# Kernel optimization log

Hardware: AMD Instinct MI355X
Metric: run time of the kernel (lower is better)

The kernel has to match this reference:

```python
import jax, jax.numpy as jnp
import numpy as np

B, C = 256, 1024
EPS = 1e-5
N_LAYERS = 3


def setup_inputs() -> dict:
    key = jax.random.key(0)
    ks = jax.random.split(key, 8)
    x = jax.random.normal(ks[0], (B, C, 7, 7), dtype=jnp.float32)
    # BatchNorm affine params per layer
    bn_gamma = 1.0 + 0.1 * jax.random.normal(ks[1], (N_LAYERS, C), dtype=jnp.float32)
    bn_beta = 0.1 * jax.random.normal(ks[2], (N_LAYERS, C), dtype=jnp.float32)
    # 1x1 conv weights [layer, out_c, in_c] and biases
    conv_w = jax.random.normal(ks[3], (N_LAYERS, C, C), dtype=jnp.float32) / np.sqrt(C)
    conv_b = 0.1 * jax.random.normal(ks[4], (N_LAYERS, C), dtype=jnp.float32)
    # prediction heads: 4 directions x 3 steps, torch Linear convention W:[out,in]
    lin_w = jax.random.normal(ks[5], (4, 3, C, C), dtype=jnp.float32) / np.sqrt(C)
    lin_b = 0.1 * jax.random.normal(ks[6], (4, 3, C), dtype=jnp.float32)
    return dict(x=x, bn_gamma=bn_gamma, bn_beta=bn_beta,
                conv_w=conv_w, conv_b=conv_b, lin_w=lin_w, lin_b=lin_b)


def _contexts(x, bn_gamma, bn_beta, conv_w, conv_b):
    # gather all 25 3x3 patches: [25, B, C, 3, 3]
    h = jnp.stack([x[:, :, y:y + 3, xx:xx + 3]
                   for y in range(5) for xx in range(5)])
    for l in range(N_LAYERS):
        # BatchNorm2d (training mode): stats over batch + spatial, per patch slice
        mean = h.mean(axis=(1, 3, 4), keepdims=True)
        var = ((h - mean) ** 2).mean(axis=(1, 3, 4), keepdims=True)
        g = bn_gamma[l][None, None, :, None, None]
        b = bn_beta[l][None, None, :, None, None]
        h = (h - mean) * jax.lax.rsqrt(var + EPS) * g + b
        h = jax.nn.relu(h)
        # 1x1 conv == per-pixel matmul over channels
        h = jnp.einsum('pbchw,oc->pbohw', h, conv_w[l]) \
            + conv_b[l][None, None, :, None, None]
    # adaptive avg pool to 1x1, squeeze -> [25, B, C]
    return h.mean(axis=(3, 4))


def reference(x, bn_gamma, bn_beta, conv_w, conv_b, lin_w, lin_b):
    ctx = _contexts(x, bn_gamma, bn_beta, conv_w, conv_b)  # [25, B, C]

    def lin(c, d, s):
        return jnp.einsum('bc,oc->bo', c, lin_w[d, s]) + lin_b[d, s]

    preds = []
    for y1 in range(5):
        for x1 in range(5):
            y2, x2 = y1 + 2, x1 + 2
            c = ctx[y1 * 5 + x1]
            if y2 in (2, 3):
                for s in range(3):
                    if y2 + s + 1 > 6:
                        break
                    preds.append(lin(c, 0, s))
            if y1 in (3, 4):
                for s in range(3):
                    if y1 - (s + 1) < 0:
                        break
                    preds.append(lin(c, 1, s))
            if x2 in (2, 3):
                for s in range(3):
                    if x2 + s + 1 > 6:
                        break
                    preds.append(lin(c, 2, s))
            if x1 in (3, 4):
                for s in range(3):
                    if x1 - (s + 1) < 0:
                        break
                    preds.append(lin(c, 3, s))
    return jnp.stack(preds)  # [120, B, C]
```

## Files before the change

### kernel.cpp

```cpp
#include <hip/hip_runtime.h>
#include <hip/hip_bf16.h>
#include <stdint.h>

#define BB 256
#define CC 1024
#define NP 25
#define EPS 1e-5f

typedef __attribute__((ext_vector_type(8))) short bf16x8;
typedef __attribute__((ext_vector_type(4))) float f32x4;
typedef unsigned int u32;

#define MFMA16(A, B, C) __builtin_amdgcn_mfma_f32_16x16x32_bf16(A, B, C, 0, 0, 0)

__device__ __forceinline__ void gload16(const u32* g, u32* l)
{
  __builtin_amdgcn_global_load_lds(
      (const __attribute__((address_space(1))) u32*)g,
      (__attribute__((address_space(3))) u32*)l, 16, 0, 0);
}


__device__ __forceinline__ void head_entry(int j, int* pp, int* ww)
{
  int cnt = 0;
  for (int y1 = 0; y1 < 5; y1++)
    for (int x1 = 0; x1 < 5; x1++) {
      int p = y1 * 5 + x1;
      int y2 = y1 + 2, x2 = x1 + 2;
      if (y2 == 2 || y2 == 3)
        for (int s = 0; s < 3; s++) { if (y2 + s + 1 > 6) break; if (cnt == j) { *pp = p; *ww = 0 + s; return; } cnt++; }
      if (y1 == 3 || y1 == 4)
        for (int s = 0; s < 3; s++) { if (y1 - (s + 1) < 0) break; if (cnt == j) { *pp = p; *ww = 3 + s; return; } cnt++; }
      if (x2 == 2 || x2 == 3)
        for (int s = 0; s < 3; s++) { if (x2 + s + 1 > 6) break; if (cnt == j) { *pp = p; *ww = 6 + s; return; } cnt++; }
      if (x1 == 3 || x1 == 4)
        for (int s = 0; s < 3; s++) { if (x1 - (s + 1) < 0) break; if (cnt == j) { *pp = p; *ww = 9 + s; return; } cnt++; }
    }
}

__device__ __forceinline__ u32 rne_hi(u32 x)
{
  return (x + 0x7FFFu + ((x >> 16) & 1u)) & 0xFFFF0000u;
}

__device__ __forceinline__ u32 rne_pack(float a, float b)
{
  return (rne_hi(__float_as_uint(a)) >> 16) | rne_hi(__float_as_uint(b));
}

__device__ __forceinline__ float bflo(u32 u) { return __uint_as_float(u << 16); }
__device__ __forceinline__ float bfhi(u32 u) { return __uint_as_float(u & 0xFFFF0000u); }


__global__ void k_xsums(const float* __restrict__ x, float* __restrict__ xs1,
                        float* __restrict__ xs2)
{
  int pos = blockIdx.x * 256 + threadIdx.x;
  float s1 = 0.f, s2 = 0.f;
  for (int b = 0; b < BB; b++) {
    float v = x[(size_t)b * 50176 + pos];
    s1 += v; s2 = fmaf(v, v, s2);
  }
  xs1[pos] = s1; xs2[pos] = s2;
}

__global__ void k_stats1(const float* __restrict__ xs1, const float* __restrict__ xs2,
                         const float* __restrict__ gam, const float* __restrict__ bet,
                         float* __restrict__ ssc, float* __restrict__ ssh)
{
  int p = blockIdx.x;
  int c = blockIdx.y * 256 + threadIdx.x;
  int y1 = p / 5, x1 = p % 5;
  float s1 = 0.f, s2 = 0.f;
  for (int dy = 0; dy < 3; dy++)
    for (int dx = 0; dx < 3; dx++) {
      int pos = c * 49 + (y1 + dy) * 7 + (x1 + dx);
      s1 += xs1[pos]; s2 += xs2[pos];
    }
  const float inv = 1.0f / 2304.0f;
  float mean = s1 * inv;
  float var  = s2 * inv - mean * mean;
  float rs   = rsqrtf(var + EPS);
  float sc   = rs * gam[c];
  ssc[(size_t)p * CC + c] = sc;
  ssh[(size_t)p * CC + c] = bet[c] - mean * sc;
}


__global__ void k_tsplit(const float* __restrict__ x,
                         const float* __restrict__ ssc, const float* __restrict__ ssh,
                         u32* __restrict__ bufS, int pbase, int pcount)
{
  __shared__ float tile[128][51];
  int b = blockIdx.x, cg = blockIdx.y;
  const float* src = x + (size_t)b * 50176 + (size_t)cg * 128 * 49;
  for (int idx = threadIdx.x; idx < 6272; idx += 256)
    tile[idx / 49][idx % 49] = src[idx];
  __syncthreads();
  const int t = threadIdx.x;
  const int u = t & 63;
  const int segs = pcount * 9;
  for (int sg = t >> 6; sg < segs; sg += 4) {
    int pl = sg / 9, yx = sg - pl * 9;
    int p = pbase + pl;
    int pos = (p / 5 + yx / 3) * 7 + (p % 5) + (yx % 3);
    int c0 = cg * 128 + u * 2;
    float2 sc = *(const float2*)(ssc + (size_t)p * CC + c0);
    float2 sh = *(const float2*)(ssh + (size_t)p * CC + c0);
    float v0 = fmaxf(fmaf(tile[u * 2][pos],     sc.x, sh.x), 0.f);
    float v1 = fmaxf(fmaf(tile[u * 2 + 1][pos], sc.y, sh.y), 0.f);
    bufS[((size_t)pl * 2304 + b * 9 + yx) * 512 + cg * 64 + u] = rne_pack(v0, v1);
  }
}


__global__ void k_wsplit_rn(const float* __restrict__ w, u32* __restrict__ dst, int total)
{
  int g = blockIdx.x * 256 + threadIdx.x;
  if (g >= total) return;
  int row = g >> 9;
  int idx = g & 511;
  const float* src = w + ((size_t)row << 10) + 2 * idx;
  dst[g] = rne_pack(src[0], src[1]);
}


__global__ void k_absplit(const u32* __restrict__ src,
                          const float* __restrict__ ssc, const float* __restrict__ ssh,
                          u32* __restrict__ dst, int pbase)
{
  int r = blockIdx.x * 8 + (threadIdx.x >> 5);
  int slab = threadIdx.x & 31;
  int pg = pbase + r / 2304;
  const u32* su = src + (size_t)r * 512 + slab * 16;
  const float* scp = ssc + (size_t)pg * CC + slab * 32;
  const float* shp = ssh + (size_t)pg * CC + slab * 32;
  u32 hi[16];
  #pragma unroll
  for (int j = 0; j < 8; j++) {
    u32 p0 = su[2 * j], p1 = su[2 * j + 1];
    float4 f = { bflo(p0), bfhi(p0), bflo(p1), bfhi(p1) };
    float4 s = *(const float4*)(scp + 4 * j);
    float4 h = *(const float4*)(shp + 4 * j);
    f.x = fmaxf(fmaf(f.x, s.x, h.x), 0.f);
    f.y = fmaxf(fmaf(f.y, s.y, h.y), 0.f);
    f.z = fmaxf(fmaf(f.z, s.z, h.z), 0.f);
    f.w = fmaxf(fmaf(f.w, s.w, h.w), 0.f);
    hi[2 * j]     = rne_pack(f.x, f.y);
    hi[2 * j + 1] = rne_pack(f.z, f.w);
  }
  u32* op = dst + (size_t)r * 512 + slab * 16;
  *(uint4*)(op + 0)  = make_uint4(hi[0], hi[1], hi[2], hi[3]);
  *(uint4*)(op + 4)  = make_uint4(hi[4], hi[5], hi[6], hi[7]);
  *(uint4*)(op + 8)  = make_uint4(hi[8], hi[9], hi[10], hi[11]);
  *(uint4*)(op + 12) = make_uint4(hi[12], hi[13], hi[14], hi[15]);
}


__global__ void k_statsfin(const float* __restrict__ part, const float* __restrict__ gam,
                           const float* __restrict__ bet, float* __restrict__ ssc,
                           float* __restrict__ ssh, int pbase)
{
  int pl = blockIdx.x;
  int c  = blockIdx.y * 256 + threadIdx.x;
  float s1 = 0.f, s2 = 0.f;
  for (int mb = 0; mb < 18; mb++) {
    const float* pp = part + ((size_t)(pl * 18 + mb) * CC + c) * 2;
    s1 += pp[0]; s2 += pp[1];
  }
  const float inv = 1.0f / 2304.0f;
  float mean = s1 * inv;
  float var  = s2 * inv - mean * mean;
  float rs   = rsqrtf(var + EPS);
  float sc   = rs * gam[c];
  int pg = pbase + pl;
  ssc[(size_t)pg * CC + c] = sc;
  ssh[(size_t)pg * CC + c] = bet[c] - mean * sc;
}


__global__ void k_pool(const u32* __restrict__ h, const float* __restrict__ ssc,
                       const float* __restrict__ ssh, u32* __restrict__ apool, int pbase)
{
  int row = blockIdx.x;
  int pl = row >> 8;
  int pg = pbase + pl;
  int c = threadIdx.x * 4;
  float4 sc = *(const float4*)(ssc + (size_t)pg * CC + c);
  float4 sh = *(const float4*)(ssh + (size_t)pg * CC + c);
  const u32* hp = h + (size_t)row * 9 * 512 + (c >> 1);
  float4 s = {0.f, 0.f, 0.f, 0.f};
  #pragma unroll
  for (int yx = 0; yx < 9; yx++) {
    uint2 pp = *(const uint2*)(hp + (size_t)yx * 512);
    float4 v = { bflo(pp.x), bfhi(pp.x), bflo(pp.y), bfhi(pp.y) };
    s.x += fmaxf(fmaf(v.x, sc.x, sh.x), 0.f);
    s.y += fmaxf(fmaf(v.y, sc.y, sh.y), 0.f);
    s.z += fmaxf(fmaf(v.z, sc.z, sh.z), 0.f);
    s.w += fmaxf(fmaf(v.w, sc.w, sh.w), 0.f);
  }
  const float inv9 = 1.0f / 9.0f;
  uint2 o = { rne_pack(s.x * inv9, s.y * inv9), rne_pack(s.z * inv9, s.w * inv9) };
  u32* op = apool + ((size_t)(pbase * 256) + row) * 512 + (c >> 1);
  *(uint2*)op = o;
}


template<int OUT, bool STATS>
__device__ __forceinline__ void mg_body(
    const u32* __restrict__ Agl, const u32* __restrict__ Bp,
    const float* __restrict__ bias, void* __restrict__ Cptr,
    int m0, int n0, float* __restrict__ partOut, int mb)
{
  __shared__ u32 sA[2][128 * 16];
  __shared__ u32 sB[2][128 * 16];

  const int t = threadIdx.x;
  const int l = t & 63, wv = t >> 6;
  const int lr = l & 15, lk = l >> 4;
  const int wm = (wv >> 1) * 64, wn = (wv & 1) * 64;

  int fAh[4], fBh[4];
  #pragma unroll
  for (int i = 0; i < 4; i++) {
    int Ra = wm + i * 16 + lr;
    int Rb = wn + i * 16 + lr;
    fAh[i] = Ra * 16 + ((lk ^ ((Ra >> 1) & 3)) << 2);
    fBh[i] = Rb * 16 + ((lk ^ ((Rb >> 1) & 3)) << 2);
  }

  int grow[2], gg[2], gdst[2];
  #pragma unroll
  for (int q = 0; q < 2; q++) {
    int rr = wv * 32 + q * 16 + (l >> 2);
    grow[q] = rr;
    gg[q] = (((l & 3) ^ ((rr >> 1) & 3)) << 2);
    gdst[q] = (wv * 32 + q * 16) * 16;
  }
  const u32* Brow = Bp + (size_t)n0 * 512;
  const u32* Agr  = Agl + (size_t)m0 * 512;

  f32x4 acc[4][4];
  #pragma unroll
  for (int i = 0; i < 4; i++)
    #pragma unroll
    for (int j = 0; j < 4; j++) { f32x4 z = {0.f, 0.f, 0.f, 0.f}; acc[i][j] = z; }

  #pragma unroll
  for (int q = 0; q < 2; q++) {
    gload16(Brow + (size_t)grow[q] * 512 + gg[q], &sB[0][gdst[q]]);
    gload16(Agr + (size_t)grow[q] * 512 + gg[q], &sA[0][gdst[q]]);
  }
  __syncthreads();

  #pragma unroll 1
  for (int it = 0; it < 32; ++it) {
    const int cur = it & 1, nxt = cur ^ 1;
    const bool pf = (it < 31);
    if (pf) {
      const int so = (it + 1) << 4;
      #pragma unroll
      for (int q = 0; q < 2; q++) {
        gload16(Brow + (size_t)grow[q] * 512 + so + gg[q], &sB[nxt][gdst[q]]);
        gload16(Agr + (size_t)grow[q] * 512 + so + gg[q], &sA[nxt][gdst[q]]);
      }
    }
    bf16x8 Ah[4], Bh[4];
    #pragma unroll
    for (int i = 0; i < 4; i++) {
      Ah[i] = *(const bf16x8*)&sA[cur][fAh[i]];
      Bh[i] = *(const bf16x8*)&sB[cur][fBh[i]];
    }
    #pragma unroll
    for (int i = 0; i < 4; i++)
      #pragma unroll
      for (int j = 0; j < 4; j++)
        acc[i][j] = MFMA16(Ah[i], Bh[j], acc[i][j]);
    __syncthreads();
  }

  float* Cf = (float*)Cptr;
  u32*   Cu = (u32*)Cptr;
  float st1[4], st2[4];
  #pragma unroll
  for (int j = 0; j < 4; j++) { st1[j] = 0.f; st2[j] = 0.f; }
  #pragma unroll
  for (int j = 0; j < 4; j++) {
    int ocol = n0 + wn + j * 16 + lr;
    float bj = bias[ocol];
    #pragma unroll
    for (int i = 0; i < 4; i++) {
      int orow = m0 + wm + i * 16 + lk * 4;
      #pragma unroll
      for (int reg = 0; reg < 4; reg++) {
        float v = acc[i][j][reg] + bj;
        if (STATS) { st1[j] += v; st2[j] = fmaf(v, v, st2[j]); }
        int row = orow + reg;
        if (OUT == 0) {
          Cf[(size_t)row * CC + ocol] = v;
        } else {
          float pv = __shfl_xor(v, 1);
          if (!(lr & 1))
            Cu[(size_t)row * 512 + (ocol >> 1)] = rne_pack(v, pv);
        }
      }
    }
  }
  if (STATS) {
    float* srb = (float*)&sA[0][0];
    #pragma unroll
    for (int j = 0; j < 4; j++) {
      st1[j] += __shfl_xor(st1[j], 16, 64);
      st1[j] += __shfl_xor(st1[j], 32, 64);
      st2[j] += __shfl_xor(st2[j], 16, 64);
      st2[j] += __shfl_xor(st2[j], 32, 64);
    }
    if (lk == 0) {
      #pragma unroll
      for (int j = 0; j < 4; j++) {
        srb[wv * 64 + j * 16 + lr]       = st1[j];
        srb[256 + wv * 64 + j * 16 + lr] = st2[j];
      }
    }
    __syncthreads();
    if (t < 128) {
      int ch = t >> 6, c6 = t & 63;
      float a1 = srb[ch * 64 + c6] + srb[(ch + 2) * 64 + c6];
      float a2 = srb[256 + ch * 64 + c6] + srb[256 + (ch + 2) * 64 + c6];
      float2 o = { a1, a2 };
      *(float2*)(partOut + ((size_t)mb * CC + n0 + t) * 2) = o;
    }
  }
}

#define SWZ_G 64

template<int OUT, bool STATS>
__global__ __launch_bounds__(256, 2)
void k_mg(const u32* __restrict__ A, const u32* __restrict__ Bp,
          const float* __restrict__ bias, void* __restrict__ Cptr,
          int mtiles, float* __restrict__ partOut)
{
  int id = blockIdx.y * gridDim.x + blockIdx.x;
  int g = id / (SWZ_G * 8);
  int rem = id - g * (SWZ_G * 8);
  int gsz = mtiles - g * SWZ_G; if (gsz > SWZ_G) gsz = SWZ_G;
  int mt = g * SWZ_G + rem % gsz;
  int nt = rem / gsz;
  mg_body<OUT, STATS>(A, Bp, bias, Cptr, mt * 128, nt * 128, partOut, mt);
}

__global__ __launch_bounds__(256, 2)
void k_heads(const u32* __restrict__ ctxp, const u32* __restrict__ wplh,
             const float* __restrict__ lb, float* __restrict__ out)
{
  int p, w;
  head_entry(blockIdx.y, &p, &w);
  mg_body<0, false>(ctxp + (size_t)p * BB * 512,
                    wplh + (size_t)w * 524288,
                    lb + (size_t)w * CC,
                    out + (size_t)blockIdx.y * BB * CC,
                    (blockIdx.x >> 3) * 128, (blockIdx.x & 7) * 128,
                    nullptr, 0);
}


extern "C" void kernel_launch(void* const* d_in, const int* in_sizes, int n_in,
                              void* d_out, int out_size, void* d_ws, size_t ws_size,
                              hipStream_t stream)
{
  const float* x   = (const float*)d_in[0];
  const float* bng = (const float*)d_in[1];
  const float* bnb = (const float*)d_in[2];
  const float* cw  = (const float*)d_in[3];
  const float* cb  = (const float*)d_in[4];
  const float* lw  = (const float*)d_in[5];
  const float* lb  = (const float*)d_in[6];
  float* out = (float*)d_out;

  const size_t W = ws_size / 4;
  const size_t SZ_WHI  = 3ull * 524288;
  const size_t SZ_WPL  = 12ull * 524288;
  const size_t SZ_PS   = 6400ull * 512;
  const size_t SZ_CTXP = 6400ull * 512;
  const size_t SZ_XS   = 50176;
  const size_t SZ_SS   = 25ull * 1024;

  auto need = [&](int pc) -> size_t {
    return SZ_WHI + SZ_WPL
         + 2ull * pc * 2304 * 512
         + SZ_PS + SZ_CTXP + 2 * SZ_XS + 2 * SZ_SS
         + (size_t)pc * 18 * 1024 * 2;
  };
  int PC;
  if      (W >= need(25)) PC = 25;
  else if (W >= need(5))  PC = 5;
  else                    PC = 1;

  u32*   whi    = (u32*)d_ws;
  u32*   wpl    = whi + SZ_WHI;
  u32*   bufS   = wpl + SZ_WPL;
  u32*   bufO   = bufS + (size_t)PC * 2304 * 512;
  u32*   pooledS= bufO + (size_t)PC * 2304 * 512;
  u32*   ctxp   = pooledS + SZ_PS;
  float* xs1    = (float*)(ctxp + SZ_CTXP);
  float* xs2    = xs1 + SZ_XS;
  float* ssc    = xs2 + SZ_XS;
  float* ssh    = ssc + SZ_SS;
  float* part   = ssh + SZ_SS;

  k_wsplit_rn<<<(int)(SZ_WHI / 256), 256, 0, stream>>>(cw, whi, (int)SZ_WHI);
  k_wsplit_rn<<<(int)(SZ_WPL / 256), 256, 0, stream>>>(lw, wpl, (int)SZ_WPL);
  k_xsums<<<196, 256, 0, stream>>>(x, xs1, xs2);
  k_stats1<<<dim3(25, 4), 256, 0, stream>>>(xs1, xs2, bng, bnb, ssc, ssh);

  for (int pbase = 0; pbase < NP; pbase += PC) {
    const int rows = PC * 2304;
    const int mtiles = PC * 18;
    const dim3 gconv(mtiles, 8);
    k_tsplit<<<dim3(256, 8), 256, 0, stream>>>(x, ssc, ssh, bufS, pbase, PC);
    k_mg<1, true><<<gconv, 256, 0, stream>>>(bufS, whi, cb, bufO, mtiles, part);
    k_statsfin<<<dim3(PC, 4), 256, 0, stream>>>(part, bng + CC, bnb + CC, ssc, ssh, pbase);
    k_absplit<<<rows / 8, 256, 0, stream>>>(bufO, ssc, ssh, bufS, pbase);
    k_mg<1, true><<<gconv, 256, 0, stream>>>(bufS, whi + 524288, cb + CC,
                                             bufO, mtiles, part);
    k_statsfin<<<dim3(PC, 4), 256, 0, stream>>>(part, bng + 2 * CC, bnb + 2 * CC, ssc, ssh, pbase);
    k_pool<<<PC * 256, 256, 0, stream>>>(bufO, ssc, ssh, pooledS, pbase);
  }

  k_mg<1, false><<<dim3(50, 8), 256, 0, stream>>>(pooledS, whi + 2 * 524288,
                                                  cb + 2 * CC, ctxp, 50, nullptr);
  k_heads<<<dim3(16, 120), 256, 0, stream>>>(ctxp, wpl, lb, out);
}
```

Measured before the change: 635.2 us.

## Enlarge conv GEMM tile to 256x128 with 512-thread blocks

Replaces the 128x128 conv GEMM kernel with a 512-thread, 8-wave variant that covers 256 rows per block. Each B (weight) tile loaded into LDS is now reused across twice as many A rows, which cuts weight traffic and halves the number of blocks. The BatchNorm partial-statistics reduction is rewritten to sum over four M-waves, and `k_statsfin` now reads 9 partials per patch instead of 18. The heads GEMM keeps the old 128x128 body. The trade-offs are a larger LDS footprint per block, fewer blocks to fill the GPU, and register pressure from `launch_bounds(512,4)`.

```diff
diff --git a/kernel.cpp b/kernel.cpp
--- a/kernel.cpp
+++ b/kernel.cpp
@@ -165,8 +165,8 @@
   int pl = blockIdx.x;
   int c  = blockIdx.y * 256 + threadIdx.x;
   float s1 = 0.f, s2 = 0.f;
-  for (int mb = 0; mb < 18; mb++) {
-    const float* pp = part + ((size_t)(pl * 18 + mb) * CC + c) * 2;
+  for (int mb = 0; mb < 9; mb++) {
+    const float* pp = part + ((size_t)(pl * 9 + mb) * CC + c) * 2;
     s1 += pp[0]; s2 += pp[1];
   }
   const float inv = 1.0f / 2304.0f;
@@ -207,11 +207,10 @@
 }
 
 
-template<int OUT, bool STATS>
 __device__ __forceinline__ void mg_body(
     const u32* __restrict__ Agl, const u32* __restrict__ Bp,
-    const float* __restrict__ bias, void* __restrict__ Cptr,
-    int m0, int n0, float* __restrict__ partOut, int mb)
+    const float* __restrict__ bias, float* __restrict__ Cf,
+    int m0, int n0)
 {
   __shared__ u32 sA[2][128 * 16];
   __shared__ u32 sB[2][128 * 16];
@@ -229,7 +228,6 @@
     fAh[i] = Ra * 16 + ((lk ^ ((Ra >> 1) & 3)) << 2);
     fBh[i] = Rb * 16 + ((lk ^ ((Rb >> 1) & 3)) << 2);
   }
-
   int grow[2], gg[2], gdst[2];
   #pragma unroll
   for (int q = 0; q < 2; q++) {
@@ -257,8 +255,7 @@
   #pragma unroll 1
   for (int it = 0; it < 32; ++it) {
     const int cur = it & 1, nxt = cur ^ 1;
-    const bool pf = (it < 31);
-    if (pf) {
+    if (it < 31) {
       const int so = (it + 1) << 4;
       #pragma unroll
       for (int q = 0; q < 2; q++) {
@@ -280,11 +277,6 @@
     __syncthreads();
   }
 
-  float* Cf = (float*)Cptr;
-  u32*   Cu = (u32*)Cptr;
-  float st1[4], st2[4];
-  #pragma unroll
-  for (int j = 0; j < 4; j++) { st1[j] = 0.f; st2[j] = 0.f; }
   #pragma unroll
   for (int j = 0; j < 4; j++) {
     int ocol = n0 + wn + j * 16 + lr;
@@ -293,17 +285,116 @@
     for (int i = 0; i < 4; i++) {
       int orow = m0 + wm + i * 16 + lk * 4;
       #pragma unroll
+      for (int reg = 0; reg < 4; reg++)
+        Cf[(size_t)(orow + reg) * CC + ocol] = acc[i][j][reg] + bj;
+    }
+  }
+}
+
+__global__ __launch_bounds__(256, 2)
+void k_heads(const u32* __restrict__ ctxp, const u32* __restrict__ wplh,
+             const float* __restrict__ lb, float* __restrict__ out)
+{
+  int p, w;
+  head_entry(blockIdx.y, &p, &w);
+  mg_body(ctxp + (size_t)p * BB * 512,
+          wplh + (size_t)w * 524288,
+          lb + (size_t)w * CC,
+          out + (size_t)blockIdx.y * BB * CC,
+          (blockIdx.x >> 3) * 128, (blockIdx.x & 7) * 128);
+}
+
+
+template<bool STATS>
+__device__ __forceinline__ void mgc_body(
+    const u32* __restrict__ Agl, const u32* __restrict__ Bp,
+    const float* __restrict__ bias, u32* __restrict__ Cu,
+    int m0, int n0, float* __restrict__ partOut, int mb)
+{
+  __shared__ u32 sA[2][256 * 16];
+  __shared__ u32 sB[2][128 * 16];
+
+  const int t = threadIdx.x;
+  const int l = t & 63, wv = t >> 6;
+  const int lr = l & 15, lk = l >> 4;
+  const int wm = (wv >> 1) * 64, wn = (wv & 1) * 64;
+
+  int fAh[4], fBh[4];
+  #pragma unroll
+  for (int i = 0; i < 4; i++) {
+    int Ra = wm + i * 16 + lr;
+    int Rb = wn + i * 16 + lr;
+    fAh[i] = Ra * 16 + ((lk ^ ((Ra >> 1) & 3)) << 2);
+    fBh[i] = Rb * 16 + ((lk ^ ((Rb >> 1) & 3)) << 2);
+  }
+  int arow[2], ag[2], adst[2];
+  #pragma unroll
+  for (int q = 0; q < 2; q++) {
+    int rr = wv * 32 + q * 16 + (l >> 2);
+    arow[q] = rr;
+    ag[q] = (((l & 3) ^ ((rr >> 1) & 3)) << 2);
+    adst[q] = (wv * 32 + q * 16) * 16;
+  }
+  int brr = wv * 16 + (l >> 2);
+  int bg = (((l & 3) ^ ((brr >> 1) & 3)) << 2);
+  int bdst = (wv * 16) * 16;
+
+  const u32* Brow = Bp + (size_t)n0 * 512;
+  const u32* Agr  = Agl + (size_t)m0 * 512;
+
+  f32x4 acc[4][4];
+  #pragma unroll
+  for (int i = 0; i < 4; i++)
+    #pragma unroll
+    for (int j = 0; j < 4; j++) { f32x4 z = {0.f, 0.f, 0.f, 0.f}; acc[i][j] = z; }
+
+  gload16(Brow + (size_t)brr * 512 + bg, &sB[0][bdst]);
+  #pragma unroll
+  for (int q = 0; q < 2; q++)
+    gload16(Agr + (size_t)arow[q] * 512 + ag[q], &sA[0][adst[q]]);
+  __syncthreads();
+
+  #pragma unroll 1
+  for (int it = 0; it < 32; ++it) {
+    const int cur = it & 1, nxt = cur ^ 1;
+    if (it < 31) {
+      const int so = (it + 1) << 4;
+      gload16(Brow + (size_t)brr * 512 + so + bg, &sB[nxt][bdst]);
+      #pragma unroll
+      for (int q = 0; q < 2; q++)
+        gload16(Agr + (size_t)arow[q] * 512 + so + ag[q], &sA[nxt][adst[q]]);
+    }
+    bf16x8 Ah[4], Bh[4];
+    #pragma unroll
+    for (int i = 0; i < 4; i++) {
+      Ah[i] = *(const bf16x8*)&sA[cur][fAh[i]];
+      Bh[i] = *(const bf16x8*)&sB[cur][fBh[i]];
+    }
+    #pragma unroll
+    for (int i = 0; i < 4; i++)
+      #pragma unroll
+      for (int j = 0; j < 4; j++)
+        acc[i][j] = MFMA16(Ah[i], Bh[j], acc[i][j]);
+    __syncthreads();
+  }
+
+  float st1[4], st2[4];
+  #pragma unroll
+  for (int j = 0; j < 4; j++) { st1[j] = 0.f; st2[j] = 0.f; }
+  #pragma unroll
+  for (int j = 0; j < 4; j++) {
+    int ocol = n0 + wn + j * 16 + lr;
+    float bj = bias[ocol];
+    #pragma unroll
+    for (int i = 0; i < 4; i++) {
+      int orow = m0 + wm + i * 16 + lk * 4;
+      #pragma unroll
       for (int reg = 0; reg < 4; reg++) {
         float v = acc[i][j][reg] + bj;
         if (STATS) { st1[j] += v; st2[j] = fmaf(v, v, st2[j]); }
-        int row = orow + reg;
-        if (OUT == 0) {
-          Cf[(size_t)row * CC + ocol] = v;
-        } else {
-          float pv = __shfl_xor(v, 1);
-          if (!(lr & 1))
-            Cu[(size_t)row * 512 + (ocol >> 1)] = rne_pack(v, pv);
-        }
+        float pv = __shfl_xor(v, 1);
+        if (!(lr & 1))
+          Cu[(size_t)(orow + reg) * 512 + (ocol >> 1)] = rne_pack(v, pv);
       }
     }
   }
@@ -320,14 +411,18 @@
       #pragma unroll
       for (int j = 0; j < 4; j++) {
         srb[wv * 64 + j * 16 + lr]       = st1[j];
-        srb[256 + wv * 64 + j * 16 + lr] = st2[j];
+        srb[512 + wv * 64 + j * 16 + lr] = st2[j];
       }
     }
     __syncthreads();
     if (t < 128) {
-      int ch = t >> 6, c6 = t & 63;
-      float a1 = srb[ch * 64 + c6] + srb[(ch + 2) * 64 + c6];
-      float a2 = srb[256 + ch * 64 + c6] + srb[256 + (ch + 2) * 64 + c6];
+      int par = t >> 6, c6 = t & 63;
+      float a1 = 0.f, a2 = 0.f;
+      #pragma unroll
+      for (int k = 0; k < 4; k++) {
+        a1 += srb[(2 * k + par) * 64 + c6];
+        a2 += srb[512 + (2 * k + par) * 64 + c6];
+      }
       float2 o = { a1, a2 };
       *(float2*)(partOut + ((size_t)mb * CC + n0 + t) * 2) = o;
     }
@@ -336,11 +431,11 @@
 
 #define SWZ_G 64
 
-template<int OUT, bool STATS>
-__global__ __launch_bounds__(256, 2)
-void k_mg(const u32* __restrict__ A, const u32* __restrict__ Bp,
-          const float* __restrict__ bias, void* __restrict__ Cptr,
-          int mtiles, float* __restrict__ partOut)
+template<bool STATS>
+__global__ __launch_bounds__(512, 4)
+void k_mgc(const u32* __restrict__ A, const u32* __restrict__ Bp,
+           const float* __restrict__ bias, u32* __restrict__ Cu,
+           int mtiles, float* __restrict__ partOut)
 {
   int id = blockIdx.y * gridDim.x + blockIdx.x;
   int g = id / (SWZ_G * 8);
@@ -348,21 +443,7 @@
   int gsz = mtiles - g * SWZ_G; if (gsz > SWZ_G) gsz = SWZ_G;
   int mt = g * SWZ_G + rem % gsz;
   int nt = rem / gsz;
-  mg_body<OUT, STATS>(A, Bp, bias, Cptr, mt * 128, nt * 128, partOut, mt);
-}
-
-__global__ __launch_bounds__(256, 2)
-void k_heads(const u32* __restrict__ ctxp, const u32* __restrict__ wplh,
-             const float* __restrict__ lb, float* __restrict__ out)
-{
-  int p, w;
-  head_entry(blockIdx.y, &p, &w);
-  mg_body<0, false>(ctxp + (size_t)p * BB * 512,
-                    wplh + (size_t)w * 524288,
-                    lb + (size_t)w * CC,
-                    out + (size_t)blockIdx.y * BB * CC,
-                    (blockIdx.x >> 3) * 128, (blockIdx.x & 7) * 128,
-                    nullptr, 0);
+  mgc_body<STATS>(A, Bp, bias, Cu, mt * 256, nt * 128, partOut, mt);
 }
 
 
@@ -391,7 +472,7 @@
     return SZ_WHI + SZ_WPL
          + 2ull * pc * 2304 * 512
          + SZ_PS + SZ_CTXP + 2 * SZ_XS + 2 * SZ_SS
-         + (size_t)pc * 18 * 1024 * 2;
+         + (size_t)pc * 9 * 1024 * 2;
   };
   int PC;
   if      (W >= need(25)) PC = 25;
@@ -417,19 +498,19 @@
 
   for (int pbase = 0; pbase < NP; pbase += PC) {
     const int rows = PC * 2304;
-    const int mtiles = PC * 18;
+    const int mtiles = PC * 9;
     const dim3 gconv(mtiles, 8);
     k_tsplit<<<dim3(256, 8), 256, 0, stream>>>(x, ssc, ssh, bufS, pbase, PC);
-    k_mg<1, true><<<gconv, 256, 0, stream>>>(bufS, whi, cb, bufO, mtiles, part);
+    k_mgc<true><<<gconv, 512, 0, stream>>>(bufS, whi, cb, bufO, mtiles, part);
     k_statsfin<<<dim3(PC, 4), 256, 0, stream>>>(part, bng + CC, bnb + CC, ssc, ssh, pbase);
     k_absplit<<<rows / 8, 256, 0, stream>>>(bufO, ssc, ssh, bufS, pbase);
-    k_mg<1, true><<<gconv, 256, 0, stream>>>(bufS, whi + 524288, cb + CC,
-                                             bufO, mtiles, part);
+    k_mgc<true><<<gconv, 512, 0, stream>>>(bufS, whi + 524288, cb + CC,
+                                           bufO, mtiles, part);
     k_statsfin<<<dim3(PC, 4), 256, 0, stream>>>(part, bng + 2 * CC, bnb + 2 * CC, ssc, ssh, pbase);
     k_pool<<<PC * 256, 256, 0, stream>>>(bufO, ssc, ssh, pooledS, pbase);
   }
 
-  k_mg<1, false><<<dim3(50, 8), 256, 0, stream>>>(pooledS, whi + 2 * 524288,
-                                                  cb + 2 * CC, ctxp, 50, nullptr);
+  k_mgc<false><<<dim3(25, 8), 512, 0, stream>>>(pooledS, whi + 2 * 524288,
+                                                cb + 2 * CC, ctxp, 25, nullptr);
   k_heads<<<dim3(16, 120), 256, 0, stream>>>(ctxp, wpl, lb, out);
 }
```

New measurement: 644.7 us. Within noise of the previous version (+1.5%).
